# Performance work log

Hardware: AMD Instinct MI355X
Metric: run time of the kernel (lower is better)

The kernel has to match this reference:

```python
import jax, jax.numpy as jnp
import numpy as np

N_HEADS = 16


def sparsemax(z):
    """Sparsemax along the last axis (Martins & Astudillo 2016)."""
    S = z.shape[-1]
    z_sorted = -jnp.sort(-z, axis=-1)                      # descending
    cs = jnp.cumsum(z_sorted, axis=-1)
    k = jnp.arange(1, S + 1, dtype=z.dtype)
    support = (1.0 + k * z_sorted) > cs                    # bool mask of support
    k_z = jnp.sum(support.astype(jnp.int32), axis=-1, keepdims=True)  # support size >=1
    cs_k = jnp.take_along_axis(cs, k_z - 1, axis=-1)
    tau = (cs_k - 1.0) / k_z.astype(z.dtype)
    return jnp.maximum(z - tau, 0.0)


def setup_inputs() -> dict:
    key = jax.random.key(0)
    ks = jax.random.split(key, 5)
    B, S, D = 4, 1024, 1024
    scale = 1.0 / np.sqrt(D).astype(np.float32)
    return {
        "x": jax.random.normal(ks[0], (B, S, D), jnp.float32),
        "Wq": jax.random.normal(ks[1], (D, D), jnp.float32) * scale,
        "bq": jnp.zeros((D,), jnp.float32),
        "Wk": jax.random.normal(ks[2], (D, D), jnp.float32) * scale,
        "bk": jnp.zeros((D,), jnp.float32),
        "Wv": jax.random.normal(ks[3], (D, D), jnp.float32) * scale,
        "bv": jnp.zeros((D,), jnp.float32),
        "Wo": jax.random.normal(ks[4], (D, D), jnp.float32) * scale,
        "bo": jnp.zeros((D,), jnp.float32),
    }


def reference(x, Wq, bq, Wk, bk, Wv, bv, Wo, bo):
    B, S, D = x.shape
    H = N_HEADS
    dh = D // H
    q = x @ Wq + bq                                        # (B,S,D)
    k = x @ Wk + bk
    v = x @ Wv + bv
    # split to heads: (B,H,S,dh)
    qh = q.reshape(B, S, H, dh).transpose(0, 2, 1, 3)
    kh = k.reshape(B, S, H, dh).transpose(0, 2, 1, 3)
    logits = jnp.einsum("bhqd,bhkd->bhqk", qh, kh) / np.sqrt(dh).astype(np.float32)
    probs = sparsemax(logits)                              # (B,H,S,S)
    # shared V: mean over head components, replicated per head
    v_shared = v.reshape(B, S, H, dh).mean(axis=2)         # (B,S,dh)
    out_h = jnp.einsum("bhqk,bkd->bhqd", probs, v_shared)  # (B,H,S,dh)
    x_out = out_h.transpose(0, 2, 1, 3).reshape(B, S, D) @ Wo + bo
    avg_attention = probs.mean(axis=1)                     # (B,S,S)
    return (x_out, avg_attention)
```

## Files before the change

kernel.cpp:

```cpp
#include <hip/hip_runtime.h>

#define B_  4
#define S_  1024
#define D_  1024
#define H_  16
#define DH  64
#define BS  4096

typedef __bf16 bf16x8 __attribute__((ext_vector_type(8)));
typedef float  f32x4  __attribute__((ext_vector_type(4)));

__device__ __forceinline__ unsigned short f2bf(float f) {
    __bf16 b = (__bf16)f;
    return __builtin_bit_cast(unsigned short, b);
}
__device__ __forceinline__ float bf2f(unsigned short u) {
    return (float)__builtin_bit_cast(__bf16, u);
}
__device__ __forceinline__ void glds16(const void* g, void* l) {
    __builtin_amdgcn_global_load_lds((const __attribute__((address_space(1))) void*)g,
                                     (__attribute__((address_space(3))) void*)l, 16, 0, 0);
}

__global__ __launch_bounds__(256) void prep2(const float* __restrict__ Wq,
                                             const float* __restrict__ Wk,
                                             const float* __restrict__ Wo,
                                             const float* __restrict__ Wv,
                                             const float* __restrict__ bv,
                                             unsigned short* __restrict__ WqTh,
                                             unsigned short* __restrict__ WqTl,
                                             unsigned short* __restrict__ WkTh,
                                             unsigned short* __restrict__ WkTl,
                                             unsigned short* __restrict__ WoTh,
                                             unsigned short* __restrict__ WvTh,
                                             unsigned short* __restrict__ WvTl,
                                             float* __restrict__ bvp) {
    __shared__ float tile[32][33];
    int bid = blockIdx.x, tid = threadIdx.x;
    if (bid < 3072) {
        const float* W;
        unsigned short *Th, *Tl;
        int wantLo;
        if (bid < 1024)      { W = Wq; Th = WqTh; Tl = WqTl; wantLo = 1; }
        else if (bid < 2048) { W = Wk; Th = WkTh; Tl = WkTl; wantLo = 1; bid -= 1024; }
        else                 { W = Wo; Th = WoTh; Tl = nullptr; wantLo = 0; bid -= 2048; }
        int tn = bid & 31, tk = bid >> 5;
        int r = tid >> 3, c4 = (tid & 7) * 4;
        float4 v = *(const float4*)(W + (size_t)(tk * 32 + r) * D_ + tn * 32 + c4);
        tile[r][c4 + 0] = v.x;
        tile[r][c4 + 1] = v.y;
        tile[r][c4 + 2] = v.z;
        tile[r][c4 + 3] = v.w;
        __syncthreads();
        unsigned short hh[4], ll[4];
#pragma unroll
        for (int i = 0; i < 4; i++) {
            float f = tile[c4 + i][r];
            hh[i] = f2bf(f);
            ll[i] = f2bf(f - bf2f(hh[i]));
        }
        size_t off = (size_t)(tn * 32 + r) * D_ + tk * 32 + c4;
        *(uint2*)(Th + off) = make_uint2((unsigned)hh[0] | ((unsigned)hh[1] << 16),
                                         (unsigned)hh[2] | ((unsigned)hh[3] << 16));
        if (wantLo)
            *(uint2*)(Tl + off) = make_uint2((unsigned)ll[0] | ((unsigned)ll[1] << 16),
                                             (unsigned)ll[2] | ((unsigned)ll[3] << 16));
    } else if (bid < 3328) {
        int e = (bid - 3072) * 256 + tid;
        int d = e >> 6, j = e & 63;
        float s = 0.f;
#pragma unroll
        for (int hh = 0; hh < H_; hh++) s += Wv[(size_t)d * D_ + hh * DH + j];
        s *= (1.f / 16.f);
        unsigned short hi = f2bf(s);
        WvTh[(size_t)j * D_ + d] = hi;
        WvTl[(size_t)j * D_ + d] = f2bf(s - bf2f(hi));
        if (bid == 3072 && tid < 128) {
            float sb = 0.f;
            if (tid < 64) {
#pragma unroll
                for (int hh = 0; hh < H_; hh++) sb += bv[hh * DH + tid];
                sb *= (1.f / 16.f);
            }
            bvp[tid] = sb;
        }
    } else {
        int e = (bid - 3328) * 256 + tid;
        int row = 64 + (e >> 10), col = e & 1023;
        WvTh[(size_t)row * D_ + col] = 0;
        WvTl[(size_t)row * D_ + col] = 0;
    }
}

__global__ __launch_bounds__(256) void projg(const float* __restrict__ x,
                                             const unsigned short* __restrict__ WqTh, const unsigned short* __restrict__ WqTl,
                                             const unsigned short* __restrict__ WkTh, const unsigned short* __restrict__ WkTl,
                                             const unsigned short* __restrict__ WvTh, const unsigned short* __restrict__ WvTl,
                                             const float* __restrict__ bq, const float* __restrict__ bk,
                                             const float* __restrict__ bvp,
                                             unsigned short* __restrict__ qh, unsigned short* __restrict__ ql,
                                             unsigned short* __restrict__ kh, unsigned short* __restrict__ kl,
                                             float* __restrict__ vshb) {
    __shared__ unsigned short AhS[128 * 32];
    __shared__ unsigned short AlS[128 * 32];
    __shared__ unsigned short BhS[128 * 32];
    __shared__ unsigned short BlS[128 * 32];

    int tid = threadIdx.x, w = tid >> 6, lane = tid & 63;
    int m16 = lane & 15, qd = lane >> 4;
    int bn = blockIdx.x, bm = blockIdx.y;

    const unsigned short *Bh, *Bl;
    const float* bias;
    int mode;
    if (bn < 8)       { Bh = WqTh + (size_t)bn * 128 * D_;       Bl = WqTl + (size_t)bn * 128 * D_;       bias = bq + bn * 128;       mode = 0; }
    else if (bn < 16) { Bh = WkTh + (size_t)(bn - 8) * 128 * D_; Bl = WkTl + (size_t)(bn - 8) * 128 * D_; bias = bk + (bn - 8) * 128; mode = 1; }
    else              { Bh = WvTh; Bl = WvTl; bias = bvp; mode = 2; }

    int l4 = lane >> 2, c8 = (lane & 3) * 8;
    int rh = (w >> 1) * 64, chh = (w & 1) * 64;

    f32x4 acc[4][4];
#pragma unroll
    for (int it = 0; it < 4; it++)
#pragma unroll
        for (int jt = 0; jt < 4; jt++) acc[it][jt] = (f32x4){0.f, 0.f, 0.f, 0.f};

    int ra = tid >> 1, ca = (tid & 1) * 16;

    for (int k0 = 0; k0 < D_; k0 += 32) {
        const float* ax = x + (size_t)(bm * 128 + ra) * D_ + k0 + ca;
        float4 f0 = *(const float4*)(ax + 0);
        float4 f1 = *(const float4*)(ax + 4);
        float4 f2 = *(const float4*)(ax + 8);
        float4 f3 = *(const float4*)(ax + 12);
        __syncthreads();
        {
            float vv[16] = {f0.x, f0.y, f0.z, f0.w, f1.x, f1.y, f1.z, f1.w,
                            f2.x, f2.y, f2.z, f2.w, f3.x, f3.y, f3.z, f3.w};
            unsigned int hw[8], lw[8];
#pragma unroll
            for (int i = 0; i < 8; i++) {
                unsigned short h0 = f2bf(vv[2 * i]), h1 = f2bf(vv[2 * i + 1]);
                unsigned short l0 = f2bf(vv[2 * i] - bf2f(h0));
                unsigned short l1 = f2bf(vv[2 * i + 1] - bf2f(h1));
                hw[i] = (unsigned)h0 | ((unsigned)h1 << 16);
                lw[i] = (unsigned)l0 | ((unsigned)l1 << 16);
            }
            char* ah = (char*)AhS + ra * 64 + ca * 2;
            char* al = (char*)AlS + ra * 64 + ca * 2;
            *(uint4*)(ah + 0)  = make_uint4(hw[0], hw[1], hw[2], hw[3]);
            *(uint4*)(ah + 16) = make_uint4(hw[4], hw[5], hw[6], hw[7]);
            *(uint4*)(al + 0)  = make_uint4(lw[0], lw[1], lw[2], lw[3]);
            *(uint4*)(al + 16) = make_uint4(lw[4], lw[5], lw[6], lw[7]);
        }
        {
            const unsigned short* gbh = Bh + (size_t)(w * 32 + l4) * D_ + k0 + c8;
            const unsigned short* gbl = Bl + (size_t)(w * 32 + l4) * D_ + k0 + c8;
            glds16(gbh,                     (char*)BhS + w * 2048);
            glds16(gbh + (size_t)16 * D_,   (char*)BhS + w * 2048 + 1024);
            glds16(gbl,                     (char*)BlS + w * 2048);
            glds16(gbl + (size_t)16 * D_,   (char*)BlS + w * 2048 + 1024);
        }
        __syncthreads();
        bf16x8 ah[4], al[4], bh[4], bl[4];
#pragma unroll
        for (int it = 0; it < 4; it++) {
            ah[it] = *(const bf16x8*)((char*)AhS + (rh + it * 16 + m16) * 64 + qd * 16);
            al[it] = *(const bf16x8*)((char*)AlS + (rh + it * 16 + m16) * 64 + qd * 16);
        }
#pragma unroll
        for (int jt = 0; jt < 4; jt++) {
            bh[jt] = *(const bf16x8*)((char*)BhS + (chh + jt * 16 + m16) * 64 + qd * 16);
            bl[jt] = *(const bf16x8*)((char*)BlS + (chh + jt * 16 + m16) * 64 + qd * 16);
        }
#pragma unroll
        for (int it = 0; it < 4; it++)
#pragma unroll
            for (int jt = 0; jt < 4; jt++) {
                acc[it][jt] = __builtin_amdgcn_mfma_f32_16x16x32_bf16(ah[it], bh[jt], acc[it][jt], 0, 0, 0);
                acc[it][jt] = __builtin_amdgcn_mfma_f32_16x16x32_bf16(ah[it], bl[jt], acc[it][jt], 0, 0, 0);
                acc[it][jt] = __builtin_amdgcn_mfma_f32_16x16x32_bf16(al[it], bh[jt], acc[it][jt], 0, 0, 0);
            }
    }
#pragma unroll
    for (int it = 0; it < 4; it++)
#pragma unroll
        for (int jt = 0; jt < 4; jt++)
#pragma unroll
            for (int r = 0; r < 4; r++) {
                int R = bm * 128 + rh + it * 16 + qd * 4 + r;
                int c = chh + jt * 16 + m16;
                float v = acc[it][jt][r] + bias[c];
                if (mode == 0) {
                    v *= 0.125f;
                    unsigned short h0 = f2bf(v);
                    qh[(size_t)R * D_ + bn * 128 + c] = h0;
                    ql[(size_t)R * D_ + bn * 128 + c] = f2bf(v - bf2f(h0));
                } else if (mode == 1) {
                    unsigned short h0 = f2bf(v);
                    kh[(size_t)R * D_ + (bn - 8) * 128 + c] = h0;
                    kl[(size_t)R * D_ + (bn - 8) * 128 + c] = f2bf(v - bf2f(h0));
                } else {
                    if (c < 64) vshb[(size_t)R * 64 + c] = v;
                }
            }
}

__global__ __launch_bounds__(256) void outg(const unsigned short* __restrict__ A,
                                            const unsigned short* __restrict__ Bh,
                                            const float* __restrict__ bias,
                                            float* __restrict__ C) {
    __shared__ unsigned short AhS[128 * 32];
    __shared__ unsigned short BhS[128 * 32];

    int tid = threadIdx.x, w = tid >> 6, lane = tid & 63;
    int m16 = lane & 15, qd = lane >> 4;
    int bn = blockIdx.x, bm = blockIdx.y;
    int l4 = lane >> 2, c8 = (lane & 3) * 8;
    int rh = (w >> 1) * 64, chh = (w & 1) * 64;

    f32x4 acc[4][4];
#pragma unroll
    for (int it = 0; it < 4; it++)
#pragma unroll
        for (int jt = 0; jt < 4; jt++) acc[it][jt] = (f32x4){0.f, 0.f, 0.f, 0.f};

    for (int k0 = 0; k0 < D_; k0 += 32) {
        __syncthreads();
        {
            const unsigned short* ga = A + (size_t)(bm * 128 + w * 32 + l4) * D_ + k0 + c8;
            glds16(ga,                   (char*)AhS + w * 2048);
            glds16(ga + (size_t)16 * D_, (char*)AhS + w * 2048 + 1024);
            const unsigned short* gb = Bh + (size_t)(bn * 128 + w * 32 + l4) * D_ + k0 + c8;
            glds16(gb,                   (char*)BhS + w * 2048);
            glds16(gb + (size_t)16 * D_, (char*)BhS + w * 2048 + 1024);
        }
        __syncthreads();
        bf16x8 ah[4], bh[4];
#pragma unroll
        for (int it = 0; it < 4; it++)
            ah[it] = *(const bf16x8*)((char*)AhS + (rh + it * 16 + m16) * 64 + qd * 16);
#pragma unroll
        for (int jt = 0; jt < 4; jt++)
            bh[jt] = *(const bf16x8*)((char*)BhS + (chh + jt * 16 + m16) * 64 + qd * 16);
#pragma unroll
        for (int it = 0; it < 4; it++)
#pragma unroll
            for (int jt = 0; jt < 4; jt++)
                acc[it][jt] = __builtin_amdgcn_mfma_f32_16x16x32_bf16(ah[it], bh[jt], acc[it][jt], 0, 0, 0);
    }
#pragma unroll
    for (int it = 0; it < 4; it++)
#pragma unroll
        for (int jt = 0; jt < 4; jt++)
#pragma unroll
            for (int r = 0; r < 4; r++) {
                int R = bm * 128 + rh + it * 16 + qd * 4 + r;
                int cc = bn * 128 + chh + jt * 16 + m16;
                C[(size_t)R * D_ + cc] = acc[it][jt][r] + bias[cc];
            }
}

#define CCAP 48
__global__ __launch_bounds__(256, 4) void attn8(const unsigned short* __restrict__ qh,
                                                const unsigned short* __restrict__ ql,
                                                const unsigned short* __restrict__ kh,
                                                const unsigned short* __restrict__ kl,
                                                const float* __restrict__ vsh,
                                                unsigned short* __restrict__ och,
                                                unsigned short* __restrict__ sidx,
                                                unsigned short* __restrict__ sval,
                                                int* __restrict__ scnt) {
    __shared__ __align__(16) char KST[32768];
    __shared__ float smM[4][16];
    __shared__ float smS[4][16], smC[4][16];
    __shared__ float tau0s[16];
    __shared__ float taus[16];
    __shared__ int   ccnt[16];
    __shared__ int   ovfAny;
    __shared__ int   scnt16[16];

    float (*candV)[CCAP] = (float (*)[CCAP])(KST);
    short (*candI)[CCAP] = (short (*)[CCAP])(KST + 3072);
    float (*slotV)[16]   = (float (*)[16])(KST + 4608);
    short (*slotI)[16]   = (short (*)[16])(KST + 5632);

    int tid = threadIdx.x, w = tid >> 6, lane = tid & 63;
    int m16 = lane & 15, qd = lane >> 4;

    int bid = blockIdx.x;
    int xcd = bid & 7;
    int j   = bid >> 3;
    int bh  = ((j >> 6) << 3) | xcd;
    int qt  = j & 63;
    int bb  = bh >> 4, h = bh & 15;
    int row0g = bb * S_ + qt * 16;
    int kbase = bb * S_;

    bf16x8 aH[2], aL[2];
#pragma unroll
    for (int c = 0; c < 2; c++) {
        size_t off = (size_t)(row0g + m16) * D_ + h * DH + c * 32 + qd * 8;
        aH[c] = *(const bf16x8*)(qh + off);
        aL[c] = *(const bf16x8*)(ql + off);
    }

    f32x4 Cfr[16];
#pragma unroll
    for (int t = 0; t < 16; t++) Cfr[t] = (f32x4){0.f, 0.f, 0.f, 0.f};

    char* myK = KST + w * 8192;
    {
        int sr = lane >> 3;
        int sc = (lane & 7) ^ sr;
        const unsigned short* ksh = kh + (size_t)(kbase + w * 256 + sr) * D_ + h * DH + sc * 8;
        const unsigned short* ksl = kl + (size_t)(kbase + w * 256 + sr) * D_ + h * DH + sc * 8;

#define STAGE_K(t, buf) do {                                        \
        size_t o_ = (size_t)(t) * 16 * D_;                          \
        char* db_ = myK + (buf) * 4096;                             \
        glds16(ksh + o_,                  db_);                     \
        glds16(ksh + o_ + (size_t)8 * D_, db_ + 1024);              \
        glds16(ksl + o_,                  db_ + 2048);              \
        glds16(ksl + o_ + (size_t)8 * D_, db_ + 3072);              \
    } while (0)

        int sw0 = m16 * 128 + (((qd    ) ^ (m16 & 7)) << 4);
        int sw1 = m16 * 128 + (((4 + qd) ^ (m16 & 7)) << 4);

        STAGE_K(0, 0);
        asm volatile("s_waitcnt vmcnt(0)" ::: "memory");
        __builtin_amdgcn_sched_barrier(0);

#pragma unroll
        for (int t = 0; t < 16; t++) {
            if (t < 15) {
                STAGE_K(t + 1, (t + 1) & 1);
                asm volatile("s_waitcnt vmcnt(4)" ::: "memory");
            } else {
                asm volatile("s_waitcnt vmcnt(0)" ::: "memory");
            }
            __builtin_amdgcn_sched_barrier(0);
            const char* tbuf = myK + (t & 1) * 4096;
            bf16x8 bfh0 = *(const bf16x8*)(tbuf + sw0);
            bf16x8 bfh1 = *(const bf16x8*)(tbuf + sw1);
            bf16x8 bfl0 = *(const bf16x8*)(tbuf + 2048 + sw0);
            bf16x8 bfl1 = *(const bf16x8*)(tbuf + 2048 + sw1);
            f32x4 a = Cfr[t];
            a = __builtin_amdgcn_mfma_f32_16x16x32_bf16(aH[0], bfh0, a, 0, 0, 0);
            a = __builtin_amdgcn_mfma_f32_16x16x32_bf16(aH[1], bfh1, a, 0, 0, 0);
            a = __builtin_amdgcn_mfma_f32_16x16x32_bf16(aH[0], bfl0, a, 0, 0, 0);
            a = __builtin_amdgcn_mfma_f32_16x16x32_bf16(aH[1], bfl1, a, 0, 0, 0);
            a = __builtin_amdgcn_mfma_f32_16x16x32_bf16(aL[0], bfh0, a, 0, 0, 0);
            a = __builtin_amdgcn_mfma_f32_16x16x32_bf16(aL[1], bfh1, a, 0, 0, 0);
            Cfr[t] = a;
        }
#undef STAGE_K
    }

    float mxr[4];
#pragma unroll
    for (int r = 0; r < 4; r++) mxr[r] = -3.0e38f;
#pragma unroll
    for (int t = 0; t < 16; t++)
#pragma unroll
        for (int r = 0; r < 4; r++) mxr[r] = fmaxf(mxr[r], Cfr[t][r]);
#pragma unroll
    for (int off = 8; off >= 1; off >>= 1)
#pragma unroll
        for (int r = 0; r < 4; r++) mxr[r] = fmaxf(mxr[r], __shfl_xor(mxr[r], off, 16));
    if (m16 == 0)
#pragma unroll
        for (int r = 0; r < 4; r++) smM[w][qd * 4 + r] = mxr[r];
    if (tid < 16) ccnt[tid] = 0;
    if (tid == 0) ovfAny = 0;
    __syncthreads();
    if (tid < 16)
        tau0s[tid] = fmaxf(fmaxf(smM[0][tid], smM[1][tid]), fmaxf(smM[2][tid], smM[3][tid])) - 1.0f;
    __syncthreads();

#pragma unroll
    for (int t = 0; t < 16; t++)
#pragma unroll
        for (int r = 0; r < 4; r++) {
            float z = Cfr[t][r];
            int row = qd * 4 + r;
            if (z > tau0s[row]) {
                int pos = atomicAdd(&ccnt[row], 1);
                if (pos < CCAP) {
                    candV[row][pos] = z;
                    candI[row][pos] = (short)(w * 256 + t * 16 + m16);
                }
            }
        }
    __syncthreads();
    if (tid < 16 && ccnt[tid] > CCAP) ovfAny = 1;

    int prow = tid >> 4, pc = tid & 15;
    int nc = ccnt[prow];
    float tau = tau0s[prow];
    float z0 = -3.0e38f, z1 = -3.0e38f, z2 = -3.0e38f;
    if (nc <= CCAP) {
        z0 = (pc < nc)      ? candV[prow][pc]      : -3.0e38f;
        z1 = (pc + 16 < nc) ? candV[prow][pc + 16] : -3.0e38f;
        z2 = (pc + 32 < nc) ? candV[prow][pc + 32] : -3.0e38f;
        for (int it = 0; it < CCAP; it++) {
            float s = 0.f, c = 0.f;
            if (z0 > tau) { s += z0; c += 1.f; }
            if (z1 > tau) { s += z1; c += 1.f; }
            if (z2 > tau) { s += z2; c += 1.f; }
#pragma unroll
            for (int off = 8; off >= 1; off >>= 1) {
                s += __shfl_xor(s, off, 16);
                c += __shfl_xor(c, off, 16);
            }
            float tnew = (s - 1.f) / c;
            if (tnew > tau) tau = tnew; else break;
        }
    }
    if (pc == 0) taus[prow] = tau;
    if (tid < 16) scnt16[tid] = 0;
    __syncthreads();

    if (!ovfAny) {
        if (z0 > tau) {
            int sl = atomicAdd(&scnt16[prow], 1);
            if (sl < 16) { slotI[prow][sl] = candI[prow][pc]; slotV[prow][sl] = z0 - tau; }
        }
        if (z1 > tau) {
            int sl = atomicAdd(&scnt16[prow], 1);
            if (sl < 16) { slotI[prow][sl] = candI[prow][pc + 16]; slotV[prow][sl] = z1 - tau; }
        }
        if (z2 > tau) {
            int sl = atomicAdd(&scnt16[prow], 1);
            if (sl < 16) { slotI[prow][sl] = candI[prow][pc + 32]; slotV[prow][sl] = z2 - tau; }
        }
        __syncthreads();
    } else {
        for (int it = 0; it < 64; it++) {
            float s[4], c[4];
#pragma unroll
            for (int r = 0; r < 4; r++) { s[r] = 0.f; c[r] = 0.f; }
#pragma unroll
            for (int t = 0; t < 16; t++)
#pragma unroll
                for (int r = 0; r < 4; r++) {
                    float z = Cfr[t][r];
                    if (z > taus[qd * 4 + r]) { s[r] += z; c[r] += 1.f; }
                }
#pragma unroll
            for (int off = 8; off >= 1; off >>= 1)
#pragma unroll
                for (int r = 0; r < 4; r++) {
                    s[r] += __shfl_xor(s[r], off, 16);
                    c[r] += __shfl_xor(c[r], off, 16);
                }
            if (m16 == 0)
#pragma unroll
                for (int r = 0; r < 4; r++) {
                    smS[w][qd * 4 + r] = s[r];
                    smC[w][qd * 4 + r] = c[r];
                }
            __syncthreads();
            int done = 1;
            if (tid < 16) {
                float S = smS[0][tid] + smS[1][tid] + smS[2][tid] + smS[3][tid];
                float C = smC[0][tid] + smC[1][tid] + smC[2][tid] + smC[3][tid];
                float tnew = (S - 1.f) / C;
                if (C > 0.f && tnew > taus[tid]) { taus[tid] = tnew; done = 0; }
            }
            if (__syncthreads_and(done)) break;
        }
#pragma unroll
        for (int t = 0; t < 16; t++)
#pragma unroll
            for (int r = 0; r < 4; r++) {
                int row = qd * 4 + r;
                float p = Cfr[t][r] - taus[row];
                if (p > 0.f) {
                    int sl = atomicAdd(&scnt16[row], 1);
                    if (sl < 16) {
                        slotI[row][sl] = (short)(w * 256 + t * 16 + m16);
                        slotV[row][sl] = p;
                    }
                }
            }
        __syncthreads();
    }

    int nsl = min(scnt16[prow], 16);
    float4 accq = make_float4(0.f, 0.f, 0.f, 0.f);
    for (int sl = 0; sl < nsl; sl++) {
        int key = slotI[prow][sl];
        float p = slotV[prow][sl];
        float4 vv = *(const float4*)(vsh + (size_t)(kbase + key) * DH + pc * 4);
        accq.x += p * vv.x;
        accq.y += p * vv.y;
        accq.z += p * vv.z;
        accq.w += p * vv.w;
    }
    {
        unsigned short b0 = f2bf(accq.x), b1 = f2bf(accq.y), b2 = f2bf(accq.z), b3 = f2bf(accq.w);
        *(uint2*)(och + (size_t)(row0g + prow) * D_ + h * DH + pc * 4) =
            make_uint2((unsigned)b0 | ((unsigned)b1 << 16), (unsigned)b2 | ((unsigned)b3 << 16));
    }
    {
        size_t base = ((size_t)(row0g + prow) * H_ + h) * 16;
        if (pc == 0) scnt[(row0g + prow) * H_ + h] = nsl;
        if (pc < nsl) {
            sidx[base + pc] = (unsigned short)slotI[prow][pc];
            sval[base + pc] = f2bf(slotV[prow][pc]);
        }
    }
}

__global__ __launch_bounds__(256) void avg_reduce(const unsigned short* __restrict__ sidx,
                                                  const unsigned short* __restrict__ sval,
                                                  const int* __restrict__ scnt,
                                                  float* __restrict__ avg) {
    __shared__ float accv[1024];
    int tid = threadIdx.x;
    int grow = blockIdx.x;
    for (int i = tid; i < 1024; i += 256) accv[i] = 0.f;
    __syncthreads();
    int h = tid >> 4, sl = tid & 15;
    int n = scnt[grow * H_ + h];
    if (sl < n) {
        size_t base = ((size_t)grow * H_ + h) * 16;
        int idx = sidx[base + sl];
        float v = bf2f(sval[base + sl]);
        atomicAdd(&accv[idx], v);
    }
    __syncthreads();
    float* dst = avg + (size_t)grow * S_;
    for (int i = tid; i < 256; i += 256) {
        float4 o;
        o.x = accv[i * 4 + 0] * 0.0625f;
        o.y = accv[i * 4 + 1] * 0.0625f;
        o.z = accv[i * 4 + 2] * 0.0625f;
        o.w = accv[i * 4 + 3] * 0.0625f;
        *(float4*)(dst + i * 4) = o;
    }
}

extern "C" void kernel_launch(void* const* d_in, const int* in_sizes, int n_in,
                              void* d_out, int out_size, void* d_ws, size_t ws_size,
                              hipStream_t stream) {
    const float* x  = (const float*)d_in[0];
    const float* Wq = (const float*)d_in[1];
    const float* bq = (const float*)d_in[2];
    const float* Wk = (const float*)d_in[3];
    const float* bk = (const float*)d_in[4];
    const float* Wv = (const float*)d_in[5];
    const float* bv = (const float*)d_in[6];
    const float* Wo = (const float*)d_in[7];
    const float* bo = (const float*)d_in[8];

    float* xout = (float*)d_out;
    float* avg  = xout + (size_t)BS * D_;

    char* ws = (char*)d_ws;
    unsigned short* qhB  = (unsigned short*)(ws + 0);
    unsigned short* qlB  = (unsigned short*)(ws + (8u << 20));
    unsigned short* khB  = (unsigned short*)(ws + (16u << 20));
    unsigned short* klB  = (unsigned short*)(ws + (24u << 20));
    unsigned short* WqTh = (unsigned short*)(ws + (32u << 20));
    unsigned short* WqTl = (unsigned short*)(ws + (34u << 20));
    unsigned short* WkTh = (unsigned short*)(ws + (36u << 20));
    unsigned short* WkTl = (unsigned short*)(ws + (38u << 20));
    unsigned short* ochB = WqTh;
    unsigned short* WoTh = (unsigned short*)(ws + (40u << 20));
    unsigned short* WvTh = (unsigned short*)(ws + (42u << 20));
    unsigned short* WvTl = (unsigned short*)(ws + (42u << 20) + (256u << 10));
    float* bvp = (float*)(ws + (42u << 20) + (512u << 10));
    float* vshb = (float*)(ws + (43u << 20));
    unsigned short* sidx = (unsigned short*)(ws + (44u << 20));
    unsigned short* sval = (unsigned short*)(ws + (46u << 20));
    int* scnt = (int*)(ws + (48u << 20));

    prep2<<<3584, 256, 0, stream>>>(Wq, Wk, Wo, Wv, bv, WqTh, WqTl, WkTh, WkTl, WoTh, WvTh, WvTl, bvp);
    projg<<<dim3(17, 32), 256, 0, stream>>>(x, WqTh, WqTl, WkTh, WkTl, WvTh, WvTl,
                                            bq, bk, bvp, qhB, qlB, khB, klB, vshb);
    attn8<<<4096, 256, 0, stream>>>(qhB, qlB, khB, klB, vshb, ochB, sidx, sval, scnt);
    avg_reduce<<<4096, 256, 0, stream>>>(sidx, sval, scnt, avg);
    outg<<<dim3(8, 32), 256, 0, stream>>>(ochB, WoTh, bo, xout);
}
```

Before: 358.9 us.

## Share staged K tiles across two query groups in attention; shrink output GEMM tiles

The attention kernel now runs 512-thread blocks covering 32 query rows. Each 256-key slice of K is staged into LDS once by four waves and read by two wave groups. This halves per-query K traffic from global memory, and a triple-buffered pipeline with a block-wide barrier each step replaces the old per-wave double buffering. The output projection GEMM moves from 128x128 to 64x64 tiles, launching four times as many blocks for better CU coverage at the cost of less operand reuse. The extra per-step __syncthreads and larger LDS footprint (about 48KB) may reduce occupancy and add synchronisation stalls.

New measurement: 384.4 us. +7.1%, slower.

```diff
diff --git a/kernel.cpp b/kernel.cpp
--- a/kernel.cpp
+++ b/kernel.cpp
@@ -211,59 +211,57 @@
                                             const unsigned short* __restrict__ Bh,
                                             const float* __restrict__ bias,
                                             float* __restrict__ C) {
-    __shared__ unsigned short AhS[128 * 32];
-    __shared__ unsigned short BhS[128 * 32];
+    __shared__ unsigned short AhS[64 * 32];
+    __shared__ unsigned short BhS[64 * 32];
 
     int tid = threadIdx.x, w = tid >> 6, lane = tid & 63;
     int m16 = lane & 15, qd = lane >> 4;
     int bn = blockIdx.x, bm = blockIdx.y;
     int l4 = lane >> 2, c8 = (lane & 3) * 8;
-    int rh = (w >> 1) * 64, chh = (w & 1) * 64;
-
-    f32x4 acc[4][4];
-#pragma unroll
-    for (int it = 0; it < 4; it++)
-#pragma unroll
-        for (int jt = 0; jt < 4; jt++) acc[it][jt] = (f32x4){0.f, 0.f, 0.f, 0.f};
+    int rh = (w >> 1) * 32, chh = (w & 1) * 32;
+
+    f32x4 acc[2][2];
+#pragma unroll
+    for (int it = 0; it < 2; it++)
+#pragma unroll
+        for (int jt = 0; jt < 2; jt++) acc[it][jt] = (f32x4){0.f, 0.f, 0.f, 0.f};
 
     for (int k0 = 0; k0 < D_; k0 += 32) {
         __syncthreads();
         {
-            const unsigned short* ga = A + (size_t)(bm * 128 + w * 32 + l4) * D_ + k0 + c8;
-            glds16(ga,                   (char*)AhS + w * 2048);
-            glds16(ga + (size_t)16 * D_, (char*)AhS + w * 2048 + 1024);
-            const unsigned short* gb = Bh + (size_t)(bn * 128 + w * 32 + l4) * D_ + k0 + c8;
-            glds16(gb,                   (char*)BhS + w * 2048);
-            glds16(gb + (size_t)16 * D_, (char*)BhS + w * 2048 + 1024);
-        }
-        __syncthreads();
-        bf16x8 ah[4], bh[4];
-#pragma unroll
-        for (int it = 0; it < 4; it++)
+            const unsigned short* ga = A + (size_t)(bm * 64 + w * 16 + l4) * D_ + k0 + c8;
+            glds16(ga, (char*)AhS + w * 1024);
+            const unsigned short* gb = Bh + (size_t)(bn * 64 + w * 16 + l4) * D_ + k0 + c8;
+            glds16(gb, (char*)BhS + w * 1024);
+        }
+        __syncthreads();
+        bf16x8 ah[2], bh[2];
+#pragma unroll
+        for (int it = 0; it < 2; it++)
             ah[it] = *(const bf16x8*)((char*)AhS + (rh + it * 16 + m16) * 64 + qd * 16);
 #pragma unroll
-        for (int jt = 0; jt < 4; jt++)
+        for (int jt = 0; jt < 2; jt++)
             bh[jt] = *(const bf16x8*)((char*)BhS + (chh + jt * 16 + m16) * 64 + qd * 16);
 #pragma unroll
-        for (int it = 0; it < 4; it++)
-#pragma unroll
-            for (int jt = 0; jt < 4; jt++)
+        for (int it = 0; it < 2; it++)
+#pragma unroll
+            for (int jt = 0; jt < 2; jt++)
                 acc[it][jt] = __builtin_amdgcn_mfma_f32_16x16x32_bf16(ah[it], bh[jt], acc[it][jt], 0, 0, 0);
     }
 #pragma unroll
-    for (int it = 0; it < 4; it++)
-#pragma unroll
-        for (int jt = 0; jt < 4; jt++)
+    for (int it = 0; it < 2; it++)
+#pragma unroll
+        for (int jt = 0; jt < 2; jt++)
 #pragma unroll
             for (int r = 0; r < 4; r++) {
-                int R = bm * 128 + rh + it * 16 + qd * 4 + r;
-                int cc = bn * 128 + chh + jt * 16 + m16;
+                int R = bm * 64 + rh + it * 16 + qd * 4 + r;
+                int cc = bn * 64 + chh + jt * 16 + m16;
                 C[(size_t)R * D_ + cc] = acc[it][jt][r] + bias[cc];
             }
 }
 
 #define CCAP 48
-__global__ __launch_bounds__(256, 4) void attn8(const unsigned short* __restrict__ qh,
+__global__ __launch_bounds__(512, 4) void attn8(const unsigned short* __restrict__ qh,
                                                 const unsigned short* __restrict__ ql,
                                                 const unsigned short* __restrict__ kh,
                                                 const unsigned short* __restrict__ kl,
@@ -272,36 +270,38 @@
                                                 unsigned short* __restrict__ sidx,
                                                 unsigned short* __restrict__ sval,
                                                 int* __restrict__ scnt) {
-    __shared__ __align__(16) char KST[32768];
-    __shared__ float smM[4][16];
-    __shared__ float smS[4][16], smC[4][16];
-    __shared__ float tau0s[16];
-    __shared__ float taus[16];
-    __shared__ int   ccnt[16];
+    __shared__ __align__(16) char KST[49152];
+    __shared__ float smM[8][16];
+    __shared__ float smS[8][16], smC[8][16];
+    __shared__ float tau0s[32];
+    __shared__ float taus[32];
+    __shared__ int   ccnt[32];
     __shared__ int   ovfAny;
-    __shared__ int   scnt16[16];
+    __shared__ int   scnt16[32];
 
     float (*candV)[CCAP] = (float (*)[CCAP])(KST);
-    short (*candI)[CCAP] = (short (*)[CCAP])(KST + 3072);
-    float (*slotV)[16]   = (float (*)[16])(KST + 4608);
-    short (*slotI)[16]   = (short (*)[16])(KST + 5632);
+    short (*candI)[CCAP] = (short (*)[CCAP])(KST + 6144);
+    float (*slotV)[16]   = (float (*)[16])(KST + 9216);
+    short (*slotI)[16]   = (short (*)[16])(KST + 11264);
 
     int tid = threadIdx.x, w = tid >> 6, lane = tid & 63;
     int m16 = lane & 15, qd = lane >> 4;
+    int g  = w >> 2;
+    int ks = w & 3;
 
     int bid = blockIdx.x;
     int xcd = bid & 7;
     int j   = bid >> 3;
-    int bh  = ((j >> 6) << 3) | xcd;
-    int qt  = j & 63;
+    int bh  = ((j >> 5) << 3) | xcd;
+    int qt  = j & 31;
     int bb  = bh >> 4, h = bh & 15;
-    int row0g = bb * S_ + qt * 16;
+    int row0g = bb * S_ + qt * 32;
     int kbase = bb * S_;
 
     bf16x8 aH[2], aL[2];
 #pragma unroll
     for (int c = 0; c < 2; c++) {
-        size_t off = (size_t)(row0g + m16) * D_ + h * DH + c * 32 + qd * 8;
+        size_t off = (size_t)(row0g + g * 16 + m16) * D_ + h * DH + c * 32 + qd * 8;
         aH[c] = *(const bf16x8*)(qh + off);
         aL[c] = *(const bf16x8*)(ql + off);
     }
@@ -310,12 +310,12 @@
 #pragma unroll
     for (int t = 0; t < 16; t++) Cfr[t] = (f32x4){0.f, 0.f, 0.f, 0.f};
 
-    char* myK = KST + w * 8192;
+    char* myK = KST + ks * 12288;
     {
         int sr = lane >> 3;
         int sc = (lane & 7) ^ sr;
-        const unsigned short* ksh = kh + (size_t)(kbase + w * 256 + sr) * D_ + h * DH + sc * 8;
-        const unsigned short* ksl = kl + (size_t)(kbase + w * 256 + sr) * D_ + h * DH + sc * 8;
+        const unsigned short* ksh = kh + (size_t)(kbase + ks * 256 + sr) * D_ + h * DH + sc * 8;
+        const unsigned short* ksl = kl + (size_t)(kbase + ks * 256 + sr) * D_ + h * DH + sc * 8;
 
 #define STAGE_K(t, buf) do {                                        \
         size_t o_ = (size_t)(t) * 16 * D_;                          \
@@ -329,20 +329,22 @@
         int sw0 = m16 * 128 + (((qd    ) ^ (m16 & 7)) << 4);
         int sw1 = m16 * 128 + (((4 + qd) ^ (m16 & 7)) << 4);
 
-        STAGE_K(0, 0);
+        if (w < 4) {
+            STAGE_K(0, 0);
+            STAGE_K(1, 1);
+        }
         asm volatile("s_waitcnt vmcnt(0)" ::: "memory");
         __builtin_amdgcn_sched_barrier(0);
 
 #pragma unroll
         for (int t = 0; t < 16; t++) {
-            if (t < 15) {
-                STAGE_K(t + 1, (t + 1) & 1);
-                asm volatile("s_waitcnt vmcnt(4)" ::: "memory");
-            } else {
-                asm volatile("s_waitcnt vmcnt(0)" ::: "memory");
-            }
+            if (w < 4) {
+                if (t < 15) asm volatile("s_waitcnt vmcnt(4)" ::: "memory");
+                else        asm volatile("s_waitcnt vmcnt(0)" ::: "memory");
+            }
+            __syncthreads();
             __builtin_amdgcn_sched_barrier(0);
-            const char* tbuf = myK + (t & 1) * 4096;
+            const char* tbuf = myK + (t % 3) * 4096;
             bf16x8 bfh0 = *(const bf16x8*)(tbuf + sw0);
             bf16x8 bfh1 = *(const bf16x8*)(tbuf + sw1);
             bf16x8 bfl0 = *(const bf16x8*)(tbuf + 2048 + sw0);
@@ -355,6 +357,7 @@
             a = __builtin_amdgcn_mfma_f32_16x16x32_bf16(aL[0], bfh0, a, 0, 0, 0);
             a = __builtin_amdgcn_mfma_f32_16x16x32_bf16(aL[1], bfh1, a, 0, 0, 0);
             Cfr[t] = a;
+            if (w < 4 && t + 2 <= 15) STAGE_K(t + 2, (t + 2) % 3);
         }
 #undef STAGE_K
     }
@@ -373,11 +376,14 @@
     if (m16 == 0)
 #pragma unroll
         for (int r = 0; r < 4; r++) smM[w][qd * 4 + r] = mxr[r];
-    if (tid < 16) ccnt[tid] = 0;
+    if (tid < 32) ccnt[tid] = 0;
     if (tid == 0) ovfAny = 0;
     __syncthreads();
-    if (tid < 16)
-        tau0s[tid] = fmaxf(fmaxf(smM[0][tid], smM[1][tid]), fmaxf(smM[2][tid], smM[3][tid])) - 1.0f;
+    if (tid < 32) {
+        int gg = tid >> 4, ii = tid & 15;
+        tau0s[tid] = fmaxf(fmaxf(smM[gg * 4 + 0][ii], smM[gg * 4 + 1][ii]),
+                           fmaxf(smM[gg * 4 + 2][ii], smM[gg * 4 + 3][ii])) - 1.0f;
+    }
     __syncthreads();
 
 #pragma unroll
@@ -385,17 +391,17 @@
 #pragma unroll
         for (int r = 0; r < 4; r++) {
             float z = Cfr[t][r];
-            int row = qd * 4 + r;
+            int row = g * 16 + qd * 4 + r;
             if (z > tau0s[row]) {
                 int pos = atomicAdd(&ccnt[row], 1);
                 if (pos < CCAP) {
                     candV[row][pos] = z;
-                    candI[row][pos] = (short)(w * 256 + t * 16 + m16);
+                    candI[row][pos] = (short)(ks * 256 + t * 16 + m16);
                 }
             }
         }
     __syncthreads();
-    if (tid < 16 && ccnt[tid] > CCAP) ovfAny = 1;
+    if (tid < 32 && ccnt[tid] > CCAP) ovfAny = 1;
 
     int prow = tid >> 4, pc = tid & 15;
     int nc = ccnt[prow];
@@ -420,7 +426,7 @@
         }
     }
     if (pc == 0) taus[prow] = tau;
-    if (tid < 16) scnt16[tid] = 0;
+    if (tid < 32) scnt16[tid] = 0;
     __syncthreads();
 
     if (!ovfAny) {
@@ -447,7 +453,7 @@
 #pragma unroll
                 for (int r = 0; r < 4; r++) {
                     float z = Cfr[t][r];
-                    if (z > taus[qd * 4 + r]) { s[r] += z; c[r] += 1.f; }
+                    if (z > taus[g * 16 + qd * 4 + r]) { s[r] += z; c[r] += 1.f; }
                 }
 #pragma unroll
             for (int off = 8; off >= 1; off >>= 1)
@@ -464,9 +470,10 @@
                 }
             __syncthreads();
             int done = 1;
-            if (tid < 16) {
-                float S = smS[0][tid] + smS[1][tid] + smS[2][tid] + smS[3][tid];
-                float C = smC[0][tid] + smC[1][tid] + smC[2][tid] + smC[3][tid];
+            if (tid < 32) {
+                int gg = tid >> 4, ii = tid & 15;
+                float S = smS[gg * 4 + 0][ii] + smS[gg * 4 + 1][ii] + smS[gg * 4 + 2][ii] + smS[gg * 4 + 3][ii];
+                float C = smC[gg * 4 + 0][ii] + smC[gg * 4 + 1][ii] + smC[gg * 4 + 2][ii] + smC[gg * 4 + 3][ii];
                 float tnew = (S - 1.f) / C;
                 if (C > 0.f && tnew > taus[tid]) { taus[tid] = tnew; done = 0; }
             }
@@ -476,12 +483,12 @@
         for (int t = 0; t < 16; t++)
 #pragma unroll
             for (int r = 0; r < 4; r++) {
-                int row = qd * 4 + r;
+                int row = g * 16 + qd * 4 + r;
                 float p = Cfr[t][r] - taus[row];
                 if (p > 0.f) {
                     int sl = atomicAdd(&scnt16[row], 1);
                     if (sl < 16) {
-                        slotI[row][sl] = (short)(w * 256 + t * 16 + m16);
+                        slotI[row][sl] = (short)(ks * 256 + t * 16 + m16);
                         slotV[row][sl] = p;
                     }
                 }
@@ -582,7 +589,7 @@
     prep2<<<3584, 256, 0, stream>>>(Wq, Wk, Wo, Wv, bv, WqTh, WqTl, WkTh, WkTl, WoTh, WvTh, WvTl, bvp);
     projg<<<dim3(17, 32), 256, 0, stream>>>(x, WqTh, WqTl, WkTh, WkTl, WvTh, WvTl,
                                             bq, bk, bvp, qhB, qlB, khB, klB, vshb);
-    attn8<<<4096, 256, 0, stream>>>(qhB, qlB, khB, klB, vshb, ochB, sidx, sval, scnt);
+    attn8<<<2048, 512, 0, stream>>>(qhB, qlB, khB, klB, vshb, ochB, sidx, sval, scnt);
     avg_reduce<<<4096, 256, 0, stream>>>(sidx, sval, scnt, avg);
-    outg<<<dim3(8, 32), 256, 0, stream>>>(ochB, WoTh, bo, xout);
-}
+    outg<<<dim3(16, 64), 256, 0, stream>>>(ochB, WoTh, bo, xout);
+}
```
